# Performance work log

Measured on AMD Instinct MI355X. Metric: run time of the kernel, lower is better.

## Reference

```python
import jax, jax.numpy as jnp
import numpy as np

N, K, V_FEATS, FILTERS = 50000, 20, 128, 128


def setup_inputs() -> dict:
    key = jax.random.key(0)
    ks = jax.random.split(key, 10)
    vertices = jax.random.normal(ks[0], (N, V_FEATS), dtype=jnp.float32)
    nh_indices = jax.random.randint(ks[1], (N, K), -1, N, dtype=jnp.int32)
    int_indices = jax.random.randint(ks[2], (N, K), -1, N, dtype=jnp.int32)
    nh_edges = jax.random.uniform(ks[3], (N, K), dtype=jnp.float32)
    int_edges = jax.random.uniform(ks[4], (N, K), dtype=jnp.float32)
    is_int = jax.random.randint(ks[5], (N,), 0, 2, dtype=jnp.int32)
    scale = 1.0 / np.sqrt(V_FEATS)
    Wvc = jax.random.normal(ks[6], (V_FEATS, FILTERS), dtype=jnp.float32) * scale
    Wvn_int = jax.random.normal(ks[7], (V_FEATS, FILTERS), dtype=jnp.float32) * scale
    Wvn_nh = jax.random.normal(ks[8], (V_FEATS, FILTERS), dtype=jnp.float32) * scale
    bv = jnp.zeros((FILTERS,), dtype=jnp.float32)
    return {"vertices": vertices, "nh_indices": nh_indices, "int_indices": int_indices,
            "nh_edges": nh_edges, "int_edges": int_edges, "is_int": is_int,
            "Wvc": Wvc, "Wvn_int": Wvn_int, "Wvn_nh": Wvn_nh, "bv": bv}


def _gather_agg(v_proj, indices, edges):
    # v_proj: [N, F]; indices: [N, K] (-1 = pad); edges: [N, K]
    mask = (indices != -1)[..., None].astype(v_proj.dtype)            # [N, K, 1]
    norm = jnp.maximum(jnp.sum(indices > -1, axis=1, keepdims=True), 1).astype(v_proj.dtype)  # [N, 1]
    safe_idx = jnp.where(indices < 0, 0, indices)                      # masked slots -> dummy row 0
    gathered = v_proj[safe_idx]                                        # [N, K, F]
    return jnp.sum(gathered * mask * edges[..., None], axis=1) / norm  # [N, F]


def reference(vertices, nh_indices, int_indices, nh_edges, int_edges, is_int,
              Wvc, Wvn_int, Wvn_nh, bv):
    Zc = vertices @ Wvc                                # [N, F]
    v_Wvn_int = vertices @ Wvn_int                     # [N, F]
    v_Wvn_nh = vertices @ Wvn_nh                       # [N, F]
    Zn_inter = _gather_agg(v_Wvn_int, int_indices, int_edges)
    Zn_nh = _gather_agg(v_Wvn_nh, nh_indices, nh_edges)
    z = jax.nn.relu(Zc + Zn_inter + Zn_nh + bv)        # bias=True; dropout omitted (eval)
    return (z, nh_indices, int_indices, nh_edges, int_edges, is_int)
```

## Files before the change

### kernel.cpp

```cpp
#include <hip/hip_runtime.h>

#define N_VERT 50000
#define KNBR 20
#define F 128
#define NBLK 782

typedef unsigned int uint32;
typedef unsigned short ushort16;
typedef unsigned char uint8;
typedef __attribute__((ext_vector_type(8))) short bf16x8;
typedef __attribute__((ext_vector_type(4))) float f32x4;
typedef __attribute__((ext_vector_type(2))) float f32x2;

__device__ __forceinline__ uint32 f2bf_bits(float x) {
    uint32 u = __float_as_uint(x);
    u += 0x7fff + ((u >> 16) & 1);
    return u >> 16;
}

__global__ __launch_bounds__(256) void wconv_kernel(
    const float* __restrict__ Wc, const float* __restrict__ Wi,
    const float* __restrict__ Wn, const float* __restrict__ bv,
    ushort16* __restrict__ Wt, float* __restrict__ bvp)
{
    int t = blockIdx.x * 256 + threadIdx.x;
    if (blockIdx.x == 0 && threadIdx.x < 128) {
        int c = threadIdx.x;
        bvp[c] = bv[(c & 7) * 16 + (c >> 3)];
    }
    if (t >= 3 * F * F) return;
    int w    = t >> 14;
    int r    = t & 16383;
    int kk   = r >> 12;
    int r2   = r & 4095;
    int nt   = r2 >> 9;
    int r3   = r2 & 511;
    int lane = r3 >> 3;
    int e    = r3 & 7;
    int k = kk * 32 + (lane >> 4) * 8 + e;
    int n = nt * 16 + (lane & 15);
    const float* W = (w == 0) ? Wc : ((w == 1) ? Wi : Wn);
    Wt[t] = (ushort16)f2bf_bits(W[k * F + n]);
}

__global__ __launch_bounds__(256) void mfma_proj_kernel(
    const float*    __restrict__ vert,
    const ushort16* __restrict__ Wt,
    const float*    __restrict__ bvp,
    ushort16* __restrict__ zcp,
    uint8* __restrict__ pay_i,
    uint8* __restrict__ pay_n)
{
    __shared__ uint4 wlds[32 * 64];

    const int w    = blockIdx.y;
    const int wave = threadIdx.x >> 6;
    const int lane = threadIdx.x & 63;
    const int lr   = lane & 15;
    const int lk   = lane >> 4;
    const int rb   = (blockIdx.x * 4 + wave) * 16;

    {
        const uint4* gW = (const uint4*)Wt;
        uint4 t[8];
#pragma unroll
        for (int nt = 0; nt < 8; ++nt)
            t[nt] = gW[(size_t)((w * 4 + wave) * 8 + nt) * 64 + lane];
#pragma unroll
        for (int nt = 0; nt < 8; ++nt)
            wlds[(wave * 8 + nt) * 64 + lane] = t[nt];
    }

    int rowA = rb + lr; if (rowA > N_VERT - 1) rowA = N_VERT - 1;
    const float* vrow = vert + (size_t)rowA * F;
    bf16x8 afrag[4];
#pragma unroll
    for (int kk = 0; kk < 4; ++kk) {
        const float* p = vrow + kk * 32 + lk * 8;
        f32x4 lo = *(const f32x4*)p;
        f32x4 hi = *(const f32x4*)(p + 4);
#pragma unroll
        for (int j = 0; j < 4; ++j) {
            afrag[kk][j]     = (short)f2bf_bits(lo[j]);
            afrag[kk][4 + j] = (short)f2bf_bits(hi[j]);
        }
    }

    __syncthreads();

    f32x4 acc[8];
#pragma unroll
    for (int nt = 0; nt < 8; ++nt) acc[nt] = (f32x4)(0.f);

#pragma unroll
    for (int kk = 0; kk < 4; ++kk)
#pragma unroll
        for (int nt = 0; nt < 8; ++nt) {
            bf16x8 b = *(const bf16x8*)&wlds[(kk * 8 + nt) * 64 + lane];
            acc[nt] = __builtin_amdgcn_mfma_f32_16x16x32_bf16(
                afrag[kk], b, acc[nt], 0, 0, 0);
        }

    if (w == 0) {
        f32x4 bb0 = *(const f32x4*)(bvp + lr * 8);
        f32x4 bb1 = *(const f32x4*)(bvp + lr * 8 + 4);
        float bbv[8] = {bb0[0], bb0[1], bb0[2], bb0[3], bb1[0], bb1[1], bb1[2], bb1[3]};
#pragma unroll
        for (int j = 0; j < 4; ++j) {
            int row = rb + lk * 4 + j;
            if (row >= N_VERT) continue;
            uint32 d[4];
#pragma unroll
            for (int p = 0; p < 4; ++p)
                d[p] = f2bf_bits(acc[2 * p][j] + bbv[2 * p]) |
                       (f2bf_bits(acc[2 * p + 1][j] + bbv[2 * p + 1]) << 16);
            *(uint4*)((uint8*)zcp + (size_t)row * 256 + lr * 16) =
                make_uint4(d[0], d[1], d[2], d[3]);
        }
    } else {
        uint8* pay = (w == 1) ? pay_i : pay_n;
#pragma unroll
        for (int j = 0; j < 4; ++j) {
            int row = rb + lk * 4 + j;
            if (row >= N_VERT) continue;
            uint32 lo, hi;
            lo = __builtin_amdgcn_cvt_pk_fp8_f32(acc[0][j], acc[1][j], 0, false);
            lo = __builtin_amdgcn_cvt_pk_fp8_f32(acc[2][j], acc[3][j], lo, true);
            hi = __builtin_amdgcn_cvt_pk_fp8_f32(acc[4][j], acc[5][j], 0, false);
            hi = __builtin_amdgcn_cvt_pk_fp8_f32(acc[6][j], acc[7][j], hi, true);
            *(uint2*)(pay + (size_t)row * 128 + lr * 8) = make_uint2(lo, hi);
        }
    }
}

__global__ __launch_bounds__(256) void agg_kernel(
    const uint8*  __restrict__ pay_i,
    const uint8*  __restrict__ pay_n,
    const unsigned short* __restrict__ zcp,
    const int4*   __restrict__ int_idx4,
    const int4*   __restrict__ nh_idx4,
    const float4* __restrict__ int_e4,
    const float4* __restrict__ nh_e4,
    float* __restrict__ z)
{
    const int lane = threadIdx.x & 63;
    const int wave = threadIdx.x >> 6;
    const int vg   = lane >> 4;
    const int fg   = lane & 15;
    const int i    = blockIdx.x * 16 + wave * 4 + vg;

    float a_i[8], a_n[8];
#pragma unroll
    for (int j = 0; j < 8; ++j) { a_i[j] = 0.f; a_n[j] = 0.f; }
    int ci = 0, cn = 0;

    {
        int sidx[KNBR]; float f[KNBR];
#pragma unroll
        for (int q = 0; q < 5; ++q) {
            int4   a = int_idx4[i * 5 + q];
            float4 e = int_e4[i * 5 + q];
            int   av[4] = {a.x, a.y, a.z, a.w};
            float ev[4] = {e.x, e.y, e.z, e.w};
#pragma unroll
            for (int j = 0; j < 4; ++j) {
                bool v = av[j] >= 0;
                ci += v;
                sidx[4 * q + j] = v ? av[j] : 0;
                f[4 * q + j]    = v ? ev[j] : 0.f;
            }
        }
        uint2 g[KNBR];
#pragma unroll
        for (int k = 0; k < KNBR; ++k)
            g[k] = *(const uint2*)(pay_i + (size_t)sidx[k] * 128 + fg * 8);
#pragma unroll
        for (int k = 0; k < KNBR; ++k) {
            float e = f[k];
            f32x2 p01 = __builtin_amdgcn_cvt_pk_f32_fp8((int)g[k].x, false);
            f32x2 p23 = __builtin_amdgcn_cvt_pk_f32_fp8((int)g[k].x, true);
            f32x2 p45 = __builtin_amdgcn_cvt_pk_f32_fp8((int)g[k].y, false);
            f32x2 p67 = __builtin_amdgcn_cvt_pk_f32_fp8((int)g[k].y, true);
            a_i[0] = fmaf(p01[0], e, a_i[0]);
            a_i[1] = fmaf(p01[1], e, a_i[1]);
            a_i[2] = fmaf(p23[0], e, a_i[2]);
            a_i[3] = fmaf(p23[1], e, a_i[3]);
            a_i[4] = fmaf(p45[0], e, a_i[4]);
            a_i[5] = fmaf(p45[1], e, a_i[5]);
            a_i[6] = fmaf(p67[0], e, a_i[6]);
            a_i[7] = fmaf(p67[1], e, a_i[7]);
        }
    }
    {
        int sidx[KNBR]; float f[KNBR];
#pragma unroll
        for (int q = 0; q < 5; ++q) {
            int4   a = nh_idx4[i * 5 + q];
            float4 e = nh_e4[i * 5 + q];
            int   av[4] = {a.x, a.y, a.z, a.w};
            float ev[4] = {e.x, e.y, e.z, e.w};
#pragma unroll
            for (int j = 0; j < 4; ++j) {
                bool v = av[j] >= 0;
                cn += v;
                sidx[4 * q + j] = v ? av[j] : 0;
                f[4 * q + j]    = v ? ev[j] : 0.f;
            }
        }
        uint2 g[KNBR];
#pragma unroll
        for (int k = 0; k < KNBR; ++k)
            g[k] = *(const uint2*)(pay_n + (size_t)sidx[k] * 128 + fg * 8);
#pragma unroll
        for (int k = 0; k < KNBR; ++k) {
            float e = f[k];
            f32x2 p01 = __builtin_amdgcn_cvt_pk_f32_fp8((int)g[k].x, false);
            f32x2 p23 = __builtin_amdgcn_cvt_pk_f32_fp8((int)g[k].x, true);
            f32x2 p45 = __builtin_amdgcn_cvt_pk_f32_fp8((int)g[k].y, false);
            f32x2 p67 = __builtin_amdgcn_cvt_pk_f32_fp8((int)g[k].y, true);
            a_n[0] = fmaf(p01[0], e, a_n[0]);
            a_n[1] = fmaf(p01[1], e, a_n[1]);
            a_n[2] = fmaf(p23[0], e, a_n[2]);
            a_n[3] = fmaf(p23[1], e, a_n[3]);
            a_n[4] = fmaf(p45[0], e, a_n[4]);
            a_n[5] = fmaf(p45[1], e, a_n[5]);
            a_n[6] = fmaf(p67[0], e, a_n[6]);
            a_n[7] = fmaf(p67[1], e, a_n[7]);
        }
    }

    float ri = 1.f / (float)max(ci, 1);
    float rn = 1.f / (float)max(cn, 1);

    uint4 zq = *(const uint4*)(zcp + (size_t)i * 128 + fg * 8);
    uint32 zd[4] = {zq.x, zq.y, zq.z, zq.w};
    float* zrow = z + (size_t)i * F + fg;
#pragma unroll
    for (int t = 0; t < 8; ++t) {
        uint32 dw = zd[t >> 1];
        float zc = __uint_as_float((t & 1) ? (dw & 0xffff0000u) : (dw << 16));
        float r  = zc + a_i[t] * ri + a_n[t] * rn;
        zrow[t * 16] = fmaxf(r, 0.f);
    }
}

__global__ void pass_kernel(const int*   __restrict__ nh_idx,
                            const int*   __restrict__ int_idx,
                            const float* __restrict__ nh_e,
                            const float* __restrict__ int_e,
                            const int*   __restrict__ is_int,
                            float* __restrict__ out)
{
    const size_t NK    = (size_t)N_VERT * KNBR;
    const size_t total = 4 * NK + N_VERT;
    size_t t = (size_t)blockIdx.x * blockDim.x + threadIdx.x;
    if (t >= total) return;

    float v;
    if      (t <     NK) v = (float)nh_idx[t];
    else if (t < 2 * NK) v = (float)int_idx[t - NK];
    else if (t < 3 * NK) v = nh_e[t - 2 * NK];
    else if (t < 4 * NK) v = int_e[t - 3 * NK];
    else                 v = (float)is_int[t - 4 * NK];
    out[t] = v;
}

extern "C" void kernel_launch(void* const* d_in, const int* in_sizes, int n_in,
                              void* d_out, int out_size, void* d_ws, size_t ws_size,
                              hipStream_t stream) {
    const float* vert    = (const float*)d_in[0];
    const int*   nh_idx  = (const int*)  d_in[1];
    const int*   int_idx = (const int*)  d_in[2];
    const float* nh_e    = (const float*)d_in[3];
    const float* int_e   = (const float*)d_in[4];
    const int*   is_int  = (const int*)  d_in[5];
    const float* Wc      = (const float*)d_in[6];
    const float* Wi      = (const float*)d_in[7];
    const float* Wn      = (const float*)d_in[8];
    const float* bv      = (const float*)d_in[9];

    float* z        = (float*)d_out;
    float* out_rest = z + (size_t)N_VERT * F;

    uint8* pay_i = (uint8*)d_ws;
    uint8* pay_n = pay_i + (size_t)N_VERT * F;
    ushort16* zcp = (ushort16*)(pay_n + (size_t)N_VERT * F);
    float* bvp   = (float*)(zcp + (size_t)N_VERT * F);
    ushort16* Wt = (ushort16*)(bvp + F);

    wconv_kernel<<<(3 * F * F + 255) / 256, 256, 0, stream>>>(Wc, Wi, Wn, bv, Wt, bvp);
    mfma_proj_kernel<<<dim3(NBLK, 3), 256, 0, stream>>>(
        vert, Wt, bvp, zcp, pay_i, pay_n);
    agg_kernel<<<N_VERT / 16, 256, 0, stream>>>(
        pay_i, pay_n, (const unsigned short*)zcp,
        (const int4*)int_idx, (const int4*)nh_idx,
        (const float4*)int_e, (const float4*)nh_e, z);

    const size_t total = (size_t)4 * N_VERT * KNBR + N_VERT;
    pass_kernel<<<(int)((total + 255) / 256), 256, 0, stream>>>(
        nh_idx, int_idx, nh_e, int_e, is_int, out_rest);
}
```

Measured before the change: 72.13 us.

## Fuse three projections per block and merge passthrough copy into aggregation kernel

The projection kernel now computes all three weight projections in one block, reusing the converted vertex fragments instead of reloading and reconverting them for each of three grid slices. Weights are read directly from global memory, so the LDS staging and barrier are gone. Separately, the passthrough copy of indices, edges and is_int is folded into the aggregation launch as extra grid-stride blocks, which removes one kernel launch and lets the copy overlap the gather. The trade-off is more per-thread register pressure and repeated global weight reads, which rely on L1/L2 hits.

```diff
diff --git a/kernel.cpp b/kernel.cpp
--- a/kernel.cpp
+++ b/kernel.cpp
@@ -4,6 +4,8 @@
 #define KNBR 20
 #define F 128
 #define NBLK 782
+#define AGG_BLOCKS 3125
+#define PASS_BLOCKS 1024
 
 typedef unsigned int uint32;
 typedef unsigned short ushort16;
@@ -43,7 +45,7 @@
     Wt[t] = (ushort16)f2bf_bits(W[k * F + n]);
 }
 
-__global__ __launch_bounds__(256) void mfma_proj_kernel(
+__global__ __launch_bounds__(256, 4) void mfma_proj_kernel(
     const float*    __restrict__ vert,
     const ushort16* __restrict__ Wt,
     const float*    __restrict__ bvp,
@@ -51,26 +53,12 @@
     uint8* __restrict__ pay_i,
     uint8* __restrict__ pay_n)
 {
-    __shared__ uint4 wlds[32 * 64];
-
-    const int w    = blockIdx.y;
     const int wave = threadIdx.x >> 6;
     const int lane = threadIdx.x & 63;
     const int lr   = lane & 15;
     const int lk   = lane >> 4;
     const int rb   = (blockIdx.x * 4 + wave) * 16;
 
-    {
-        const uint4* gW = (const uint4*)Wt;
-        uint4 t[8];
-#pragma unroll
-        for (int nt = 0; nt < 8; ++nt)
-            t[nt] = gW[(size_t)((w * 4 + wave) * 8 + nt) * 64 + lane];
-#pragma unroll
-        for (int nt = 0; nt < 8; ++nt)
-            wlds[(wave * 8 + nt) * 64 + lane] = t[nt];
-    }
-
     int rowA = rb + lr; if (rowA > N_VERT - 1) rowA = N_VERT - 1;
     const float* vrow = vert + (size_t)rowA * F;
     bf16x8 afrag[4];
@@ -86,49 +74,53 @@
         }
     }
 
-    __syncthreads();
-
-    f32x4 acc[8];
-#pragma unroll
-    for (int nt = 0; nt < 8; ++nt) acc[nt] = (f32x4)(0.f);
-
-#pragma unroll
-    for (int kk = 0; kk < 4; ++kk)
-#pragma unroll
-        for (int nt = 0; nt < 8; ++nt) {
-            bf16x8 b = *(const bf16x8*)&wlds[(kk * 8 + nt) * 64 + lane];
-            acc[nt] = __builtin_amdgcn_mfma_f32_16x16x32_bf16(
-                afrag[kk], b, acc[nt], 0, 0, 0);
-        }
-
-    if (w == 0) {
-        f32x4 bb0 = *(const f32x4*)(bvp + lr * 8);
-        f32x4 bb1 = *(const f32x4*)(bvp + lr * 8 + 4);
-        float bbv[8] = {bb0[0], bb0[1], bb0[2], bb0[3], bb1[0], bb1[1], bb1[2], bb1[3]};
-#pragma unroll
-        for (int j = 0; j < 4; ++j) {
-            int row = rb + lk * 4 + j;
-            if (row >= N_VERT) continue;
-            uint32 d[4];
-#pragma unroll
-            for (int p = 0; p < 4; ++p)
-                d[p] = f2bf_bits(acc[2 * p][j] + bbv[2 * p]) |
-                       (f2bf_bits(acc[2 * p + 1][j] + bbv[2 * p + 1]) << 16);
-            *(uint4*)((uint8*)zcp + (size_t)row * 256 + lr * 16) =
-                make_uint4(d[0], d[1], d[2], d[3]);
-        }
-    } else {
-        uint8* pay = (w == 1) ? pay_i : pay_n;
-#pragma unroll
-        for (int j = 0; j < 4; ++j) {
-            int row = rb + lk * 4 + j;
-            if (row >= N_VERT) continue;
-            uint32 lo, hi;
-            lo = __builtin_amdgcn_cvt_pk_fp8_f32(acc[0][j], acc[1][j], 0, false);
-            lo = __builtin_amdgcn_cvt_pk_fp8_f32(acc[2][j], acc[3][j], lo, true);
-            hi = __builtin_amdgcn_cvt_pk_fp8_f32(acc[4][j], acc[5][j], 0, false);
-            hi = __builtin_amdgcn_cvt_pk_fp8_f32(acc[6][j], acc[7][j], hi, true);
-            *(uint2*)(pay + (size_t)row * 128 + lr * 8) = make_uint2(lo, hi);
+    const uint4* gW = (const uint4*)Wt + lane;
+
+#pragma unroll
+    for (int w = 0; w < 3; ++w) {
+        f32x4 acc[8];
+#pragma unroll
+        for (int nt = 0; nt < 8; ++nt) acc[nt] = (f32x4)(0.f);
+
+#pragma unroll
+        for (int kk = 0; kk < 4; ++kk)
+#pragma unroll
+            for (int nt = 0; nt < 8; ++nt) {
+                bf16x8 b = *(const bf16x8*)(gW + (size_t)((w * 4 + kk) * 8 + nt) * 64);
+                acc[nt] = __builtin_amdgcn_mfma_f32_16x16x32_bf16(
+                    afrag[kk], b, acc[nt], 0, 0, 0);
+            }
+
+        if (w == 0) {
+            f32x4 bb0 = *(const f32x4*)(bvp + lr * 8);
+            f32x4 bb1 = *(const f32x4*)(bvp + lr * 8 + 4);
+            float bbv[8] = {bb0[0], bb0[1], bb0[2], bb0[3],
+                            bb1[0], bb1[1], bb1[2], bb1[3]};
+#pragma unroll
+            for (int j = 0; j < 4; ++j) {
+                int row = rb + lk * 4 + j;
+                if (row >= N_VERT) continue;
+                uint32 d[4];
+#pragma unroll
+                for (int p = 0; p < 4; ++p)
+                    d[p] = f2bf_bits(acc[2 * p][j] + bbv[2 * p]) |
+                           (f2bf_bits(acc[2 * p + 1][j] + bbv[2 * p + 1]) << 16);
+                *(uint4*)((uint8*)zcp + (size_t)row * 256 + lr * 16) =
+                    make_uint4(d[0], d[1], d[2], d[3]);
+            }
+        } else {
+            uint8* pay = (w == 1) ? pay_i : pay_n;
+#pragma unroll
+            for (int j = 0; j < 4; ++j) {
+                int row = rb + lk * 4 + j;
+                if (row >= N_VERT) continue;
+                uint32 lo, hi;
+                lo = __builtin_amdgcn_cvt_pk_fp8_f32(acc[0][j], acc[1][j], 0, false);
+                lo = __builtin_amdgcn_cvt_pk_fp8_f32(acc[2][j], acc[3][j], lo, true);
+                hi = __builtin_amdgcn_cvt_pk_fp8_f32(acc[4][j], acc[5][j], 0, false);
+                hi = __builtin_amdgcn_cvt_pk_fp8_f32(acc[6][j], acc[7][j], hi, true);
+                *(uint2*)(pay + (size_t)row * 128 + lr * 8) = make_uint2(lo, hi);
+            }
         }
     }
 }
@@ -141,8 +133,27 @@
     const int4*   __restrict__ nh_idx4,
     const float4* __restrict__ int_e4,
     const float4* __restrict__ nh_e4,
-    float* __restrict__ z)
+    float* __restrict__ z,
+    const int*   __restrict__ nh_idx,  const int*   __restrict__ int_idx,
+    const float* __restrict__ nh_e,    const float* __restrict__ int_e,
+    const int*   __restrict__ is_int,  float* __restrict__ out_rest)
 {
+    if (blockIdx.x >= AGG_BLOCKS) {
+        const size_t NK    = (size_t)N_VERT * KNBR;
+        const size_t total = 4 * NK + N_VERT;
+        size_t t0 = (size_t)(blockIdx.x - AGG_BLOCKS) * 256 + threadIdx.x;
+        for (size_t t = t0; t < total; t += (size_t)PASS_BLOCKS * 256) {
+            float v;
+            if      (t <     NK) v = (float)nh_idx[t];
+            else if (t < 2 * NK) v = (float)int_idx[t - NK];
+            else if (t < 3 * NK) v = nh_e[t - 2 * NK];
+            else if (t < 4 * NK) v = int_e[t - 3 * NK];
+            else                 v = (float)is_int[t - 4 * NK];
+            out_rest[t] = v;
+        }
+        return;
+    }
+
     const int lane = threadIdx.x & 63;
     const int wave = threadIdx.x >> 6;
     const int vg   = lane >> 4;
@@ -244,27 +255,6 @@
     }
 }
 
-__global__ void pass_kernel(const int*   __restrict__ nh_idx,
-                            const int*   __restrict__ int_idx,
-                            const float* __restrict__ nh_e,
-                            const float* __restrict__ int_e,
-                            const int*   __restrict__ is_int,
-                            float* __restrict__ out)
-{
-    const size_t NK    = (size_t)N_VERT * KNBR;
-    const size_t total = 4 * NK + N_VERT;
-    size_t t = (size_t)blockIdx.x * blockDim.x + threadIdx.x;
-    if (t >= total) return;
-
-    float v;
-    if      (t <     NK) v = (float)nh_idx[t];
-    else if (t < 2 * NK) v = (float)int_idx[t - NK];
-    else if (t < 3 * NK) v = nh_e[t - 2 * NK];
-    else if (t < 4 * NK) v = int_e[t - 3 * NK];
-    else                 v = (float)is_int[t - 4 * NK];
-    out[t] = v;
-}
-
 extern "C" void kernel_launch(void* const* d_in, const int* in_sizes, int n_in,
                               void* d_out, int out_size, void* d_ws, size_t ws_size,
                               hipStream_t stream) {
@@ -289,14 +279,11 @@
     ushort16* Wt = (ushort16*)(bvp + F);
 
     wconv_kernel<<<(3 * F * F + 255) / 256, 256, 0, stream>>>(Wc, Wi, Wn, bv, Wt, bvp);
-    mfma_proj_kernel<<<dim3(NBLK, 3), 256, 0, stream>>>(
+    mfma_proj_kernel<<<NBLK, 256, 0, stream>>>(
         vert, Wt, bvp, zcp, pay_i, pay_n);
-    agg_kernel<<<N_VERT / 16, 256, 0, stream>>>(
+    agg_kernel<<<AGG_BLOCKS + PASS_BLOCKS, 256, 0, stream>>>(
         pay_i, pay_n, (const unsigned short*)zcp,
         (const int4*)int_idx, (const int4*)nh_idx,
-        (const float4*)int_e, (const float4*)nh_e, z);
-
-    const size_t total = (size_t)4 * N_VERT * KNBR + N_VERT;
-    pass_kernel<<<(int)((total + 255) / 256), 256, 0, stream>>>(
+        (const float4*)int_e, (const float4*)nh_e, z,
         nh_idx, int_idx, nh_e, int_e, is_int, out_rest);
 }
```

Result: no change. 71.69 us (-0.6%).
